# Performance work log

Hardware: AMD Instinct MI355X
Metric: run time of the kernel (lower is better)

Reference implementation:

```python
import jax, jax.numpy as jnp
import numpy as np
import math

B, T, D_MODEL, D_HEAD = 4, 4096, 1024, 64


def setup_inputs() -> dict:
    key = jax.random.key(0)
    ks = jax.random.split(key, 7)
    s = 1.0 / math.sqrt(D_MODEL)
    return {
        "x": jax.random.normal(ks[0], (B, T, D_MODEL), dtype=jnp.float32),
        "wq": jax.random.normal(ks[1], (D_MODEL, D_HEAD), dtype=jnp.float32) * s,
        "bq": jnp.zeros((D_HEAD,), dtype=jnp.float32),
        "wk": jax.random.normal(ks[2], (D_MODEL, D_HEAD), dtype=jnp.float32) * s,
        "bk": jnp.zeros((D_HEAD,), dtype=jnp.float32),
        "wv": jax.random.normal(ks[3], (D_MODEL, D_HEAD), dtype=jnp.float32) * s,
        "bv": jnp.zeros((D_HEAD,), dtype=jnp.float32),
        # causal mask: True where attention is allowed
        "mask": jnp.tril(jnp.ones((T, T), dtype=bool)),
    }


def reference(x, wq, bq, wk, bk, wv, bv, mask):
    # x: [b, t, d_model]; wq/wk/wv: [d_model, d_head]
    q = x @ wq + bq  # [b, t, d_head]
    k = x @ wk + bk
    v = x @ wv + bv
    scale = 1.0 / math.sqrt(q.shape[-1])
    scores = jnp.einsum("btd,bsd->bts", q, k) * scale  # [b, t, t]
    scores = jnp.where(mask, scores, jnp.float32(-1e9))
    attn = jax.nn.softmax(scores, axis=-1)
    return jnp.einsum("bts,bsd->btd", attn, v)  # [b, t, d_head]
```

## Files before the change

### kernel.cpp

```cpp
#include <hip/hip_runtime.h>
#include <hip/hip_bf16.h>

typedef __attribute__((ext_vector_type(2)))  float f32x2;
typedef __attribute__((ext_vector_type(4)))  float f32x4;
typedef __attribute__((ext_vector_type(16))) float f32x16;
typedef __attribute__((ext_vector_type(8)))  short s16x8;
typedef __attribute__((ext_vector_type(2)))  unsigned int u32x2;
typedef __attribute__((ext_vector_type(4)))  unsigned int u32x4;
typedef __attribute__((ext_vector_type(2)))  int i32x2;

#define D_MODEL 1024
#define D_HEAD  64
#define SEQ_T   4096

__device__ __forceinline__ unsigned short f2bf(float f) {
    unsigned int u = __float_as_uint(f);
    u += 0x7fffu + ((u >> 16) & 1u);
    return (unsigned short)(u >> 16);
}

__device__ __forceinline__ unsigned int cvtpk_bf16(float lo, float hi) {
    unsigned int r;
    asm("v_cvt_pk_bf16_f32 %0, %1, %2" : "=v"(r) : "v"(lo), "v"(hi));
    return r;
}

__device__ __forceinline__ float ex2(float x) {
#if __has_builtin(__builtin_amdgcn_exp2f)
    return __builtin_amdgcn_exp2f(x);
#else
    return exp2f(x);
#endif
}

__device__ __forceinline__ void halfswap(unsigned int x,
                                         unsigned int& r0, unsigned int& r1) {
#if __has_builtin(__builtin_amdgcn_permlane32_swap)
    i32x2 r = __builtin_amdgcn_permlane32_swap((int)x, (int)x, false, false);
    r0 = (unsigned int)r[0];
    r1 = (unsigned int)r[1];
#else
    r0 = x;
    r1 = (unsigned int)__shfl_xor((int)x, 32);
#endif
}

__device__ __forceinline__ void gload_lds16(const unsigned short* g,
                                            unsigned short* l) {
#if __has_builtin(__builtin_amdgcn_global_load_lds)
    __builtin_amdgcn_global_load_lds(
        (const __attribute__((address_space(1))) void*)g,
        (__attribute__((address_space(3))) void*)l, 16, 0, 0);
#else
    const int lane = (int)(threadIdx.x & 63);
    *(u32x4*)((char*)l + lane * 16) = *(const u32x4*)g;
#endif
}

__device__ __forceinline__ f32x4 mfma16(s16x8 a, s16x8 b, f32x4 c) {
    return __builtin_amdgcn_mfma_f32_16x16x32_bf16(a, b, c, 0, 0, 0);
}
__device__ __forceinline__ f32x16 mfma32(s16x8 a, s16x8 b, f32x16 c) {
    return __builtin_amdgcn_mfma_f32_32x32x16_bf16(a, b, c, 0, 0, 0);
}

__global__ __launch_bounds__(256) void wconv_kernel(
    const float* __restrict__ wq, const float* __restrict__ wk,
    const float* __restrict__ wv, unsigned short* __restrict__ wT)
{
    int idx = blockIdx.x * 256 + threadIdx.x;
    int mat = idx >> 16;
    int rem = idx & 65535;
    int k = rem >> 6, n = rem & 63;
    const float* w = (mat == 0) ? wq : (mat == 1) ? wk : wv;
    wT[(size_t)(mat * 64 + n) * D_MODEL + k] = f2bf(w[rem]);
}

#define XB 72
__global__ __launch_bounds__(256, 2) void qkv_kernel(
    const float* __restrict__ x,
    const float* __restrict__ bq, const float* __restrict__ bk,
    const float* __restrict__ bv,
    const unsigned short* __restrict__ wT,
    unsigned short* __restrict__ q_ws, unsigned short* __restrict__ k_ws,
    unsigned short* __restrict__ vT_ws)
{
    __shared__ unsigned short xbf[2][64 * XB];
    __shared__ unsigned short wls[2][96 * 64];
    const int t = threadIdx.x;
    const int lane = t & 63, w = t >> 6;
    const int wr = w >> 1, wc = w & 1;
    const int lr = lane & 15, lg = lane >> 4;
    const int mb = (int)blockIdx.x >> 1, nb = (int)blockIdx.x & 1;

    const float* xsrc = x + (size_t)(mb * 64 + (t >> 4)) * D_MODEL + (t & 15) * 4;
    const unsigned short* wgbase = wT
        + (size_t)(nb * 96 + (lane >> 3)) * D_MODEL
        + ((lane & 7) ^ (lane >> 3)) * 8;

    f32x4 acc[2][3];
#pragma unroll
    for (int s = 0; s < 2; ++s)
#pragma unroll
        for (int c = 0; c < 3; ++c) acc[s][c] = (f32x4)0.0f;

    f32x4 xreg[4];

#define GLOADX(K0) do {                                                        \
    _Pragma("unroll") for (int j = 0; j < 4; ++j)                              \
        xreg[j] = *(const f32x4*)(xsrc + (size_t)j * 16 * D_MODEL + (K0));     \
} while (0)

#define WLOAD(BUF, K0) do {                                                    \
    _Pragma("unroll") for (int j = 0; j < 3; ++j) {                            \
        const int i = w * 3 + j;                                               \
        gload_lds16(wgbase + (size_t)(i * 8) * D_MODEL + (K0),                 \
                    &wls[BUF][i * 512]);                                       \
    }                                                                          \
} while (0)

#define DSWRITEX(BUF) do {                                                     \
    unsigned short* XP = &xbf[BUF][0];                                         \
    _Pragma("unroll") for (int j = 0; j < 4; ++j) {                            \
        u32x2 pv;                                                              \
        pv[0] = cvtpk_bf16(xreg[j][0], xreg[j][1]);                            \
        pv[1] = cvtpk_bf16(xreg[j][2], xreg[j][3]);                            \
        *(u32x2*)(XP + ((t >> 4) + j * 16) * XB + (t & 15) * 4) = pv;          \
    }                                                                          \
} while (0)

#define COMPUTE(BUF) do {                                                      \
    const unsigned short* XP = &xbf[BUF][0];                                   \
    const char* WB = (const char*)&wls[BUF][0];                                \
    _Pragma("unroll") for (int ks = 0; ks < 2; ++ks) {                         \
        s16x8 af[2];                                                           \
        _Pragma("unroll") for (int sub = 0; sub < 2; ++sub)                    \
            af[sub] = *(const s16x8*)(XP + (wr * 32 + sub * 16 + lr) * XB      \
                                      + ks * 32 + lg * 8);                     \
        _Pragma("unroll") for (int tc = 0; tc < 3; ++tc) {                     \
            const int rowR = wc * 48 + tc * 16 + lr;                           \
            const int cb = (ks * 64 + lg * 16) ^ ((rowR & 7) << 4);            \
            s16x8 bf = *(const s16x8*)(WB + rowR * 128 + cb);                  \
            acc[0][tc] = mfma16(af[0], bf, acc[0][tc]);                        \
            acc[1][tc] = mfma16(af[1], bf, acc[1][tc]);                        \
        }                                                                      \
    }                                                                          \
} while (0)

    GLOADX(0);
    WLOAD(0, 0);
    DSWRITEX(0);
    GLOADX(64);
    __syncthreads();

    for (int step = 0; step < 16; ++step) {
        const int cur = step & 1;
        if (step + 1 < 16) {
            WLOAD(cur ^ 1, (step + 1) * 64);
            DSWRITEX(cur ^ 1);
        }
        if (step + 2 < 16) GLOADX((step + 2) * 64);
        COMPUTE(cur);
        __syncthreads();
    }

#undef GLOADX
#undef WLOAD
#undef DSWRITEX
#undef COMPUTE

#pragma unroll
    for (int sub = 0; sub < 2; ++sub)
#pragma unroll
        for (int tc = 0; tc < 3; ++tc) {
            int col = nb * 96 + wc * 48 + tc * 16 + lr;
            float bias = (col < 64) ? bq[col] : (col < 128) ? bk[col - 64] : bv[col - 128];
#pragma unroll
            for (int r = 0; r < 4; ++r) {
                int row = mb * 64 + wr * 32 + sub * 16 + lg * 4 + r;
                float v = acc[sub][tc][r] + bias;
                int bb = row >> 12, tt = row & 4095;
                int cc_ = tt >> 5;
                if (col < 64) {
                    q_ws[(size_t)row * 64 + col] = f2bf(v * 0.18033688011112042f);
                } else if (col < 128) {
                    int kcol = col - 64;
                    int d = kcol >> 4, hi2 = (kcol >> 3) & 1, e = kcol & 7;
                    int l = (tt & 31) + 32 * hi2;
                    k_ws[(size_t)(((bb * 128 + cc_) * 4 + d) * 64 + l) * 8 + e] = f2bf(v);
                } else {
                    int h = col - 128;
                    int w32 = tt & 31;
                    int fb0 = (w32 >> 4) & 1, hi2 = (w32 >> 3) & 1, e = w32 & 7;
                    int f = ((h >> 5) << 1) | fb0;
                    int l = (h & 31) + 32 * hi2;
                    vT_ws[(size_t)(((bb * 128 + cc_) * 4 + f) * 64 + l) * 8 + e] = f2bf(v);
                }
            }
        }
}

__global__ __launch_bounds__(1024, 4) void attn_kernel(
    const unsigned short* __restrict__ q_ws, const unsigned short* __restrict__ k_ws,
    const unsigned short* __restrict__ vT_ws, float* __restrict__ out)
{
    __shared__ float solds[8][32][66];
    __shared__ float sml[16][2][32];
    const int lane = threadIdx.x & 63;
    const int w = threadIdx.x >> 6;
    const int q = lane & 31;
    const int hi = lane >> 5;
    const int khalf = 4 * hi;
    const int b = ((int)blockIdx.x & 7) >> 1;
    const int p = ((int)blockIdx.x >> 3) + (((int)blockIdx.x & 1) << 5);

#define PUBLISH(SLOT) do {                                                     \
    _Pragma("unroll") for (int i = 0; i < 16; ++i) {                           \
        int d = (i & 3) + 8 * (i >> 2) + khalf;                                \
        solds[SLOT][q][d] = o0[i];                                             \
        solds[SLOT][q][d + 32] = o1[i];                                        \
    }                                                                          \
    if (!hi) { sml[w][0][q] = m; sml[w][1][q] = lsum; }                        \
} while (0)

#define MERGE(SLOT, PW) do {                                                   \
    float mp = sml[PW][0][q], lp = sml[PW][1][q];                              \
    float M = fmaxf(m, mp);                                                    \
    float e = ex2(m - M), ep = ex2(mp - M);                                    \
    m = M; lsum = lsum * e + lp * ep;                                          \
    _Pragma("unroll") for (int i = 0; i < 16; ++i) {                           \
        int d = (i & 3) + 8 * (i >> 2) + khalf;                                \
        o0[i] = o0[i] * e + solds[SLOT][q][d] * ep;                            \
        o1[i] = o1[i] * e + solds[SLOT][q][d + 32] * ep;                       \
    }                                                                          \
} while (0)

    const unsigned short* kt = k_ws + (size_t)(b * 128) * 2048;
    const unsigned short* vt = vT_ws + (size_t)(b * 128) * 2048;
    const int lane8 = lane * 8;

    for (int half = 0; half < 2; ++half) {
        const int qb = (half == 0) ? p : 127 - p;
        const int q0 = SEQ_T - 32 * (qb + 1);
        const int ntiles = (q0 >> 5) + 1;

        const unsigned short* qrow = q_ws + ((size_t)(b * SEQ_T + q0 + q)) * 64 + hi * 8;
        s16x8 qf[4];
#pragma unroll
        for (int d = 0; d < 4; ++d) qf[d] = *(const s16x8*)(qrow + d * 16);

        f32x16 o0 = (f32x16)0.0f, o1 = (f32x16)0.0f;
        float m = -1e30f, lsum = 0.0f;

        int c = w;
        if (c < ntiles) {
            s16x8 kf[4];
            {
                const unsigned short* kp = kt + (size_t)c * 2048 + lane8;
#pragma unroll
                for (int d = 0; d < 4; ++d) kf[d] = *(const s16x8*)(kp + d * 512);
            }
            for (; c < ntiles; c += 16) {
                const int kv = c << 5;
                f32x16 s = (f32x16)0.0f;
                __builtin_amdgcn_s_setprio(1);
#pragma unroll
                for (int d = 0; d < 4; ++d) s = mfma32(kf[d], qf[d], s);
                __builtin_amdgcn_s_setprio(0);
                {
                    const int cn = (c + 16 < ntiles) ? c + 16 : 0;
                    const unsigned short* kp = kt + (size_t)cn * 2048 + lane8;
#pragma unroll
                    for (int d = 0; d < 4; ++d) kf[d] = *(const s16x8*)(kp + d * 512);
                }
                const unsigned short* vp = vt + (size_t)c * 2048 + lane8;
                s16x8 vf00 = *(const s16x8*)(vp);
                s16x8 vf01 = *(const s16x8*)(vp + 512);
                s16x8 vf10 = *(const s16x8*)(vp + 1024);
                s16x8 vf11 = *(const s16x8*)(vp + 1536);
                if (kv + 32 > q0) {
                    const int qg = q0 + q;
#pragma unroll
                    for (int i = 0; i < 16; ++i) {
                        int kk = kv + (i & 3) + 8 * (i >> 2) + khalf;
                        if (kk > qg) s[i] = -1e30f;
                    }
                }
                float t0, t1;
                t0 = fmaxf(s[0], s[1]);   t1 = fmaxf(s[2], s[3]);   t0 = fmaxf(t0, t1);
                t1 = fmaxf(s[4], s[5]);   t1 = fmaxf(t1, fmaxf(s[6], s[7]));
                float t2 = fmaxf(fmaxf(s[8], s[9]), fmaxf(s[10], s[11]));
                float t3 = fmaxf(fmaxf(s[12], s[13]), fmaxf(s[14], s[15]));
                float mx = fmaxf(fmaxf(t0, t1), fmaxf(t2, t3));
                {
                    unsigned int r0, r1;
                    halfswap(__float_as_uint(mx), r0, r1);
                    mx = fmaxf(__uint_as_float(r0), __uint_as_float(r1));
                }
                const float mnew = fmaxf(m, mx);
                const float corr = ex2(m - mnew);
                m = mnew;
                float rs = 0.0f;
#pragma unroll
                for (int i = 0; i < 16; ++i) {
                    float pv = ex2(s[i] - mnew);
                    s[i] = pv;
                    rs += pv;
                }
                {
                    unsigned int r0, r1;
                    halfswap(__float_as_uint(rs), r0, r1);
                    rs = __uint_as_float(r0) + __uint_as_float(r1);
                }
                lsum = lsum * corr + rs;
#pragma unroll
                for (int i = 0; i < 16; ++i) { o0[i] *= corr; o1[i] *= corr; }
                unsigned int cc[8], pc[8];
#pragma unroll
                for (int i = 0; i < 8; ++i) cc[i] = cvtpk_bf16(s[2 * i], s[2 * i + 1]);
#pragma unroll
                for (int i = 0; i < 8; ++i) {
                    unsigned int r0, r1;
                    halfswap(cc[i], r0, r1);
                    pc[i] = r0 ^ r1 ^ cc[i];
                }
                u32x4 w0, w1;
                w0[0] = hi ? pc[2] : cc[0]; w0[1] = hi ? pc[3] : cc[1];
                w0[2] = hi ? cc[2] : pc[0]; w0[3] = hi ? cc[3] : pc[1];
                w1[0] = hi ? pc[6] : cc[4]; w1[1] = hi ? pc[7] : cc[5];
                w1[2] = hi ? cc[6] : pc[4]; w1[3] = hi ? cc[7] : pc[5];
                s16x8 pb0 = __builtin_bit_cast(s16x8, w0);
                s16x8 pb1 = __builtin_bit_cast(s16x8, w1);
                __builtin_amdgcn_s_setprio(1);
                o0 = mfma32(vf00, pb0, o0);
                o0 = mfma32(vf01, pb1, o0);
                o1 = mfma32(vf10, pb0, o1);
                o1 = mfma32(vf11, pb1, o1);
                __builtin_amdgcn_s_setprio(0);
            }
        }

        if (w >= 8) PUBLISH(w - 8);
        __syncthreads();
        if (w < 8) MERGE(w, w + 8);
        __syncthreads();
        if (w >= 4 && w < 8) PUBLISH(w - 4);
        __syncthreads();
        if (w < 4) { MERGE(w, w + 4); PUBLISH(w); }
        __syncthreads();
        {
            const int qq = (int)threadIdx.x >> 5;
            const int dd = ((int)threadIdx.x & 31) * 2;
            float M = -1e30f;
#pragma unroll
            for (int ww = 0; ww < 4; ++ww) M = fmaxf(M, sml[ww][0][qq]);
            float L = 0.0f, O0 = 0.0f, O1 = 0.0f;
#pragma unroll
            for (int ww = 0; ww < 4; ++ww) {
                float e = ex2(sml[ww][0][qq] - M);
                L += sml[ww][1][qq] * e;
                O0 += solds[ww][qq][dd] * e;
                O1 += solds[ww][qq][dd + 1] * e;
            }
            f32x2 res; res[0] = O0 / L; res[1] = O1 / L;
            *(f32x2*)(out + ((size_t)(b * SEQ_T + q0 + qq)) * 64 + dd) = res;
        }
        __syncthreads();
    }
#undef PUBLISH
#undef MERGE
}

extern "C" void kernel_launch(void* const* d_in, const int* in_sizes, int n_in,
                              void* d_out, int out_size, void* d_ws, size_t ws_size,
                              hipStream_t stream) {
    const float* x  = (const float*)d_in[0];
    const float* wq = (const float*)d_in[1];
    const float* bq = (const float*)d_in[2];
    const float* wk = (const float*)d_in[3];
    const float* bk = (const float*)d_in[4];
    const float* wv = (const float*)d_in[5];
    const float* bv = (const float*)d_in[6];
    float* out = (float*)d_out;

    char* ws = (char*)d_ws;
    unsigned short* wT    = (unsigned short*)(ws);
    unsigned short* q_ws  = (unsigned short*)(ws + 393216);
    unsigned short* k_ws  = (unsigned short*)(ws + 393216 + 2097152);
    unsigned short* vT_ws = (unsigned short*)(ws + 393216 + 2 * 2097152);

    wconv_kernel<<<dim3(768), dim3(256), 0, stream>>>(wq, wk, wv, wT);
    qkv_kernel<<<dim3(512), dim3(256), 0, stream>>>(x, bq, bk, bv, wT, q_ws, k_ws, vT_ws);
    attn_kernel<<<dim3(256), dim3(1024), 0, stream>>>(q_ws, k_ws, vT_ws, out);
}
```

Before: 59.82 us.

## Stage full bf16 x tile in LDS once instead of double-buffered streaming

The QKV projection kernel now converts the block's whole 64x1024 fp32 x tile to bf16 up front. It stores it in a large chunk-major LDS array and then runs the K loop only double-buffering the weight tiles. This removes the per-step x register staging and LDS writes from the main loop. In exchange, x loading is no longer overlapped with MFMA work. Occupancy drops to one block per CU because of the ~150KB LDS footprint, and the block-to-tile mapping now separates the two column halves that share the same x rows, which may reduce L2 reuse.

```diff
diff --git a/kernel.cpp b/kernel.cpp
--- a/kernel.cpp
+++ b/kernel.cpp
@@ -76,8 +76,7 @@
     wT[(size_t)(mat * 64 + n) * D_MODEL + k] = f2bf(w[rem]);
 }
 
-#define XB 72
-__global__ __launch_bounds__(256, 2) void qkv_kernel(
+__global__ __launch_bounds__(256, 1) void qkv_kernel(
     const float* __restrict__ x,
     const float* __restrict__ bq, const float* __restrict__ bk,
     const float* __restrict__ bv,
@@ -85,31 +84,17 @@
     unsigned short* __restrict__ q_ws, unsigned short* __restrict__ k_ws,
     unsigned short* __restrict__ vT_ws)
 {
-    __shared__ unsigned short xbf[2][64 * XB];
+    __shared__ unsigned short xt[128 * 64 * 8];
     __shared__ unsigned short wls[2][96 * 64];
     const int t = threadIdx.x;
     const int lane = t & 63, w = t >> 6;
     const int wr = w >> 1, wc = w & 1;
     const int lr = lane & 15, lg = lane >> 4;
-    const int mb = (int)blockIdx.x >> 1, nb = (int)blockIdx.x & 1;
-
-    const float* xsrc = x + (size_t)(mb * 64 + (t >> 4)) * D_MODEL + (t & 15) * 4;
+    const int mb = (int)blockIdx.x & 255, nb = (int)blockIdx.x >> 8;
+
     const unsigned short* wgbase = wT
         + (size_t)(nb * 96 + (lane >> 3)) * D_MODEL
         + ((lane & 7) ^ (lane >> 3)) * 8;
-
-    f32x4 acc[2][3];
-#pragma unroll
-    for (int s = 0; s < 2; ++s)
-#pragma unroll
-        for (int c = 0; c < 3; ++c) acc[s][c] = (f32x4)0.0f;
-
-    f32x4 xreg[4];
-
-#define GLOADX(K0) do {                                                        \
-    _Pragma("unroll") for (int j = 0; j < 4; ++j)                              \
-        xreg[j] = *(const f32x4*)(xsrc + (size_t)j * 16 * D_MODEL + (K0));     \
-} while (0)
 
 #define WLOAD(BUF, K0) do {                                                    \
     _Pragma("unroll") for (int j = 0; j < 3; ++j) {                            \
@@ -119,24 +104,38 @@
     }                                                                          \
 } while (0)
 
-#define DSWRITEX(BUF) do {                                                     \
-    unsigned short* XP = &xbf[BUF][0];                                         \
-    _Pragma("unroll") for (int j = 0; j < 4; ++j) {                            \
-        u32x2 pv;                                                              \
-        pv[0] = cvtpk_bf16(xreg[j][0], xreg[j][1]);                            \
-        pv[1] = cvtpk_bf16(xreg[j][2], xreg[j][3]);                            \
-        *(u32x2*)(XP + ((t >> 4) + j * 16) * XB + (t & 15) * 4) = pv;          \
-    }                                                                          \
-} while (0)
-
-#define COMPUTE(BUF) do {                                                      \
-    const unsigned short* XP = &xbf[BUF][0];                                   \
+    WLOAD(0, 0);
+    {
+        const int row = t >> 2;
+        const float* xr = x + (size_t)(mb * 64 + row) * D_MODEL + (t & 3) * 256;
+        for (int i = 0; i < 32; ++i) {
+            f32x4 a0 = *(const f32x4*)(xr + i * 8);
+            f32x4 a1 = *(const f32x4*)(xr + i * 8 + 4);
+            u32x4 pv;
+            pv[0] = cvtpk_bf16(a0[0], a0[1]);
+            pv[1] = cvtpk_bf16(a0[2], a0[3]);
+            pv[2] = cvtpk_bf16(a1[0], a1[1]);
+            pv[3] = cvtpk_bf16(a1[2], a1[3]);
+            const int c = (t & 3) * 32 + i;
+            *(u32x4*)(xt + (c * 64 + row) * 8) = pv;
+        }
+    }
+
+    f32x4 acc[2][3];
+#pragma unroll
+    for (int s = 0; s < 2; ++s)
+#pragma unroll
+        for (int c = 0; c < 3; ++c) acc[s][c] = (f32x4)0.0f;
+
+#define COMPUTE(BUF, K0) do {                                                  \
     const char* WB = (const char*)&wls[BUF][0];                                \
     _Pragma("unroll") for (int ks = 0; ks < 2; ++ks) {                         \
         s16x8 af[2];                                                           \
-        _Pragma("unroll") for (int sub = 0; sub < 2; ++sub)                    \
-            af[sub] = *(const s16x8*)(XP + (wr * 32 + sub * 16 + lr) * XB      \
-                                      + ks * 32 + lg * 8);                     \
+        _Pragma("unroll") for (int sub = 0; sub < 2; ++sub) {                  \
+            const int ch = ((K0) >> 3) + ks * 4 + lg;                          \
+            const int rw = wr * 32 + sub * 16 + lr;                            \
+            af[sub] = *(const s16x8*)(xt + (ch * 64 + rw) * 8);                \
+        }                                                                      \
         _Pragma("unroll") for (int tc = 0; tc < 3; ++tc) {                     \
             const int rowR = wc * 48 + tc * 16 + lr;                           \
             const int cb = (ks * 64 + lg * 16) ^ ((rowR & 7) << 4);            \
@@ -147,26 +146,16 @@
     }                                                                          \
 } while (0)
 
-    GLOADX(0);
-    WLOAD(0, 0);
-    DSWRITEX(0);
-    GLOADX(64);
     __syncthreads();
 
     for (int step = 0; step < 16; ++step) {
         const int cur = step & 1;
-        if (step + 1 < 16) {
-            WLOAD(cur ^ 1, (step + 1) * 64);
-            DSWRITEX(cur ^ 1);
-        }
-        if (step + 2 < 16) GLOADX((step + 2) * 64);
-        COMPUTE(cur);
+        if (step + 1 < 16) WLOAD(cur ^ 1, (step + 1) * 64);
+        COMPUTE(cur, step * 64);
         __syncthreads();
     }
 
-#undef GLOADX
 #undef WLOAD
-#undef DSWRITEX
 #undef COMPUTE
 
 #pragma unroll
```

Result: slower. 78.12 us (+30.6%).
